# Kernel tuning notes

Measured on AMD Instinct MI355X. Metric: run time of the kernel, lower is better.

## Reference

```python
import jax, jax.numpy as jnp
import numpy as np

D_MODEL, D_K, D_V, H, GRID = 512, 64, 64, 8, 196
B = 4


def setup_inputs() -> dict:
    key = jax.random.key(0)
    ks = jax.random.split(key, 12)
    s = 0.02
    return {
        "queries": jax.random.normal(ks[0], (B, GRID, D_MODEL), jnp.float32),
        "keys": jax.random.normal(ks[1], (B, GRID, D_MODEL), jnp.float32),
        "values": jax.random.normal(ks[2], (B, GRID, D_MODEL), jnp.float32),
        "Wq": jax.random.normal(ks[3], (H * D_K, D_MODEL), jnp.float32) * s,
        "bq": jnp.zeros((H * D_K,), jnp.float32),
        "Wk": jax.random.normal(ks[4], (H * D_K, D_MODEL), jnp.float32) * s,
        "bk": jnp.zeros((H * D_K,), jnp.float32),
        "Wv": jax.random.normal(ks[5], (H * D_V, D_MODEL), jnp.float32) * s,
        "bv": jnp.zeros((H * D_V,), jnp.float32),
        "Wo": jax.random.normal(ks[6], (D_MODEL, H * D_V), jnp.float32) * s,
        "bo": jnp.zeros((D_MODEL,), jnp.float32),
        "scale": jnp.ones((1, H, GRID, GRID), jnp.float32) / np.sqrt(D_K).astype(np.float32),
    }


def reference(queries, keys, values, Wq, bq, Wk, bk, Wv, bv, Wo, bo, scale):
    b, nq, _ = queries.shape
    nk = values.shape[1]
    # linear projections (torch nn.Linear: x @ W.T + b)
    q_sig = queries @ Wq.T + bq          # (b, nq, h*dk)
    k_p = keys @ Wk.T + bk               # (b, nk, h*dk)
    v_p = values @ Wv.T + bv             # (b, nk, h*dv)
    # elementwise q*k interaction (b, nq, nk, h*dk)
    att_e = q_sig[:, :, None, :] * k_p[:, None, :, :]
    # sigmoid-gated values
    v_g = jax.nn.sigmoid(att_e) * v_p[:, None, :, :]
    v = v_g.reshape(b, nq, nk, H, D_K).transpose(0, 3, 1, 2, 4)      # (b,h,nq,nk,dk)
    att = att_e.reshape(b, nq, nk, H, D_K).transpose(0, 3, 1, 2, 4)  # (b,h,nq,nk,dk)
    att = att.sum(-1) * scale            # (b,h,nq,nk)
    p = jax.nn.softmax(att, axis=-1)     # dropout is identity in eval mode
    # (att.unsqueeze(-2) @ v).squeeze(-2)
    image = jnp.einsum("bhqk,bhqkd->bhqd", p, v)
    image = image.transpose(0, 2, 1, 3).reshape(b, nq, H * D_V)
    out = image @ Wo.T + bo              # (b, nq, d_model)
    out = jax.nn.sigmoid(q_sig * out) * out
    return out
```

## Files before the change

### kernel.cpp

```cpp
#include <hip/hip_runtime.h>
#include <hip/hip_bf16.h>
#include <math.h>

#define NQ 196
#define BATCH 4
#define HD 512
#define NH 8
#define DK 64
#define MROWS 784
#define MPAD 832

typedef __attribute__((ext_vector_type(8))) short short8;
typedef __attribute__((ext_vector_type(4))) float float4v;

__device__ __forceinline__ float b2f(short s) {
  return __uint_as_float(((unsigned)(unsigned short)s) << 16);
}
__device__ __forceinline__ short f2b(float x) {
  return __builtin_bit_cast(short, __float2bfloat16(x));
}
__device__ __forceinline__ float fexp2(float x) {
  float r; asm("v_exp_f32 %0, %1" : "=v"(r) : "v"(x)); return r;
}
__device__ __forceinline__ float frcp(float x) {
  float r; asm("v_rcp_f32 %0, %1" : "=v"(r) : "v"(x)); return r;
}

struct SplitArgs {
  const float* src[7];
  short* hi[7];
  short* lo[7];
};

__global__ __launch_bounds__(256)
void split_kernel(SplitArgs a) {
  const int blk = blockIdx.x;
  int seg, base;
  if (blk < 588) { seg = blk / 196; base = seg * 196; }
  else           { seg = 3 + (blk - 588) / 128; base = 588 + (seg - 3) * 128; }
  const size_t off = (size_t)(blk - base) * 2048 + (size_t)threadIdx.x * 8;
  const float* src = a.src[seg] + off;
  float4 v0 = *(const float4*)(src);
  float4 v1 = *(const float4*)(src + 4);
  float x[8] = {v0.x, v0.y, v0.z, v0.w, v1.x, v1.y, v1.z, v1.w};
  short hh[8], ll[8];
  #pragma unroll
  for (int i = 0; i < 8; ++i) {
    hh[i] = f2b(x[i]);
    ll[i] = f2b(x[i] - b2f(hh[i]));
  }
  short8 vh = {hh[0],hh[1],hh[2],hh[3],hh[4],hh[5],hh[6],hh[7]};
  short8 vl = {ll[0],ll[1],ll[2],ll[3],ll[4],ll[5],ll[6],ll[7]};
  *(short8*)(a.hi[seg] + off) = vh;
  *(short8*)(a.lo[seg] + off) = vl;
}

struct GemmZ {
  const short* Ah[3]; const short* Al[3];
  const short* Bh[3]; const short* Bl[3];
  const float* bias[3];
  float* Cf[3]; short* Ch[3]; short* Cl[3];
  const short* Gh; const short* Gl;
};

__global__ __launch_bounds__(256)
void mfma_gemm(GemmZ p, int M, int N, int K) {
  const int z = blockIdx.z;
  const short* __restrict__ Ah = p.Ah[z];
  const short* __restrict__ Al = p.Al[z];
  const short* __restrict__ Bh = p.Bh[z];
  const short* __restrict__ Bl = p.Bl[z];

  __shared__ short ldsA[2][2][32 * 32];
  __shared__ short ldsB[2][2][64 * 32];

  const int t = threadIdx.x;
  const int w = t >> 6, ln = t & 63;
  const int lm = ln & 15, quad = ln >> 4;
  const int m0 = blockIdx.x * 32, n0 = blockIdx.y * 64;

  const int aArr = t >> 7;
  const int aIdx = t & 127;
  const int aRow = aIdx >> 2, aK = (aIdx & 3) << 3;
  const int bRow = t >> 2,    bK = (t & 3) << 3;
  const short* __restrict__ Asrc = aArr ? Al : Ah;
  const size_t aoff = (size_t)(m0 + aRow) * K + aK;
  const size_t boff = (size_t)(n0 + bRow) * K + bK;

  const int wm = (w & 1) << 4, wn = (w >> 1) << 5;

  float4v acc[2] = {{0.f,0.f,0.f,0.f},{0.f,0.f,0.f,0.f}};

  short8 rA  = *(const short8*)(Asrc + aoff);
  short8 rBh = *(const short8*)(Bh + boff);
  short8 rBl = *(const short8*)(Bl + boff);

  const int T = K >> 5;
  for (int kt = 0; kt < T; ++kt) {
    const int buf = kt & 1;
    *(short8*)&ldsA[buf][aArr][aRow * 32 + aK] = rA;
    *(short8*)&ldsB[buf][0][bRow * 32 + bK]    = rBh;
    *(short8*)&ldsB[buf][1][bRow * 32 + bK]    = rBl;
    __syncthreads();
    if (kt + 1 < T) {
      rA  = *(const short8*)(Asrc + aoff + (size_t)(kt + 1) * 32);
      rBh = *(const short8*)(Bh + boff + (size_t)(kt + 1) * 32);
      rBl = *(const short8*)(Bl + boff + (size_t)(kt + 1) * 32);
    }
    short8 fah = *(const short8*)&ldsA[buf][0][(wm + lm) * 32 + (quad << 3)];
    short8 fal = *(const short8*)&ldsA[buf][1][(wm + lm) * 32 + (quad << 3)];
    #pragma unroll
    for (int ni = 0; ni < 2; ++ni) {
      short8 fbh = *(const short8*)&ldsB[buf][0][(wn + (ni << 4) + lm) * 32 + (quad << 3)];
      short8 fbl = *(const short8*)&ldsB[buf][1][(wn + (ni << 4) + lm) * 32 + (quad << 3)];
      acc[ni] = __builtin_amdgcn_mfma_f32_16x16x32_bf16(fah, fbh, acc[ni], 0,0,0);
      acc[ni] = __builtin_amdgcn_mfma_f32_16x16x32_bf16(fah, fbl, acc[ni], 0,0,0);
      acc[ni] = __builtin_amdgcn_mfma_f32_16x16x32_bf16(fal, fbh, acc[ni], 0,0,0);
    }
  }

  const float* bias = p.bias[z];
  float* Cf = p.Cf[z]; short* Ch = p.Ch[z]; short* Cl = p.Cl[z];
  #pragma unroll
  for (int ni = 0; ni < 2; ++ni) {
    const int n = n0 + wn + (ni << 4) + lm;
    const float bv = bias[n];
    #pragma unroll
    for (int r = 0; r < 4; ++r) {
      const int m = m0 + wm + (quad << 2) + r;
      if (m < M) {
        float c = acc[ni][r] + bv;
        if (p.Gh) {
          float qg = b2f(p.Gh[(size_t)m * N + n]) + b2f(p.Gl[(size_t)m * N + n]);
          c = __fdividef(c, 1.f + __expf(-qg * c));
        }
        if (Cf) Cf[(size_t)m * N + n] = c;
        if (Ch) {
          short hi = f2b(c);
          Ch[(size_t)m * N + n] = hi;
          Cl[(size_t)m * N + n] = f2b(c - b2f(hi));
        }
      }
    }
  }
}

__global__ __launch_bounds__(256)
void scores_softmax(const short* __restrict__ qsh, const short* __restrict__ qsl,
                    const short* __restrict__ ksh, const short* __restrict__ ksl,
                    const float* __restrict__ scg, float* __restrict__ pbuf) {
  const int q0 = blockIdx.x * 16;
  const int bh = blockIdx.y;
  const int b = bh >> 3, h = bh & 7;
  const int w = threadIdx.x >> 6, ln = threadIdx.x & 63;
  const int lm = ln & 15, quad = ln >> 4;
  const float L2E = 1.4426950408889634f;

  __shared__ float S[16][210];

  const size_t abase = ((size_t)(b * NQ) + q0 + lm) * HD + h * DK + (quad << 3);
  short8 ah0 = *(const short8*)(qsh + abase);
  short8 ah1 = *(const short8*)(qsh + abase + 32);
  short8 al0 = *(const short8*)(qsl + abase);
  short8 al1 = *(const short8*)(qsl + abase + 32);

  for (int nt = w; nt < 13; nt += 4) {
    const size_t bbase = ((size_t)(b * NQ) + nt * 16 + lm) * HD + h * DK + (quad << 3);
    short8 bh0 = *(const short8*)(ksh + bbase);
    short8 bh1 = *(const short8*)(ksh + bbase + 32);
    short8 bl0 = *(const short8*)(ksl + bbase);
    short8 bl1 = *(const short8*)(ksl + bbase + 32);
    float4v acc = {0.f, 0.f, 0.f, 0.f};
    acc = __builtin_amdgcn_mfma_f32_16x16x32_bf16(ah0, bh0, acc, 0,0,0);
    acc = __builtin_amdgcn_mfma_f32_16x16x32_bf16(ah1, bh1, acc, 0,0,0);
    acc = __builtin_amdgcn_mfma_f32_16x16x32_bf16(ah0, bl0, acc, 0,0,0);
    acc = __builtin_amdgcn_mfma_f32_16x16x32_bf16(ah1, bl1, acc, 0,0,0);
    acc = __builtin_amdgcn_mfma_f32_16x16x32_bf16(al0, bh0, acc, 0,0,0);
    acc = __builtin_amdgcn_mfma_f32_16x16x32_bf16(al1, bh1, acc, 0,0,0);
    #pragma unroll
    for (int r = 0; r < 4; ++r)
      S[(quad << 2) + r][nt * 16 + lm] = acc[r];
  }
  __syncthreads();

  for (int i = 0; i < 4; ++i) {
    const int rr = (w << 2) + i;
    const int q = q0 + rr;
    const bool qok = q < NQ;
    const float* srow = scg + ((size_t)h * NQ + (qok ? q : 0)) * NQ;
    float att[4];
    #pragma unroll
    for (int j = 0; j < 4; ++j) {
      const int c = ln + (j << 6);
      att[j] = -1e30f;
      if (c < NQ) att[j] = S[rr][c] * srow[c] * L2E;
    }
    float m = fmaxf(fmaxf(att[0], att[1]), fmaxf(att[2], att[3]));
    #pragma unroll
    for (int off = 32; off; off >>= 1) m = fmaxf(m, __shfl_xor(m, off, 64));
    float e[4], s = 0.f;
    #pragma unroll
    for (int j = 0; j < 4; ++j) { e[j] = fexp2(att[j] - m); s += e[j]; }
    #pragma unroll
    for (int off = 32; off; off >>= 1) s += __shfl_xor(s, off, 64);
    const float rinv = __fdividef(1.f, s);
    if (qok) {
      float* prow = pbuf + (((size_t)(b * NH + h) * NQ) + q) * NQ;
      #pragma unroll
      for (int j = 0; j < 4; ++j) {
        const int c = ln + (j << 6);
        if (c < NQ) prow[c] = e[j] * rinv;
      }
    }
  }
}

__global__ __launch_bounds__(512)
void pv_kernel(const short* __restrict__ qsh, const short* __restrict__ qsl,
               const float* __restrict__ kpg, const float* __restrict__ vpg,
               const float* __restrict__ pbuf, float* __restrict__ part) {
  const int b  = blockIdx.y;
  const int x  = blockIdx.x;
  const int ks = x & 3;
  const int q0 = (x >> 2) << 2;
  const int hd = threadIdx.x;
  const int h  = hd >> 6;
  const float LOG2E = 1.4426950408889634f;

  const size_t r0 = ((size_t)(b * NQ) + q0) * HD + hd;
  float nqs[4];
  #pragma unroll
  for (int qi = 0; qi < 4; ++qi) {
    const size_t rr = r0 + (size_t)qi * HD;
    nqs[qi] = -(b2f(qsh[rr]) + b2f(qsl[rr])) * LOG2E;
  }
  const float* kp = kpg + (size_t)b * NQ * HD + hd;
  const float* vp = vpg + (size_t)b * NQ * HD + hd;
  const float* pr = pbuf + ((size_t)(b * NH + h) * NQ + q0) * NQ;

  float acc[4] = {0.f, 0.f, 0.f, 0.f};
  const int kbeg = ks * 49;
  for (int k = kbeg; k < kbeg + 49; ++k) {
    const float kv = kp[(size_t)k * HD];
    const float vv = vp[(size_t)k * HD];
    #pragma unroll
    for (int qi = 0; qi < 4; ++qi) {
      const float e = fexp2(nqs[qi] * kv);
      const float g = vv * frcp(1.f + e);
      acc[qi] += pr[(size_t)qi * NQ + k] * g;
    }
  }
  float* dst = part + (size_t)ks * ((size_t)MROWS * HD) + r0;
  #pragma unroll
  for (int qi = 0; qi < 4; ++qi) dst[(size_t)qi * HD] = acc[qi];
}

__global__ __launch_bounds__(256)
void img_split(const float* __restrict__ part, short* __restrict__ ih,
               short* __restrict__ il) {
  const size_t NELF = (size_t)MROWS * HD;
  const size_t off = (size_t)blockIdx.x * 2048 + (size_t)threadIdx.x * 8;
  float x[8];
  #pragma unroll
  for (int i = 0; i < 8; i += 4) {
    float4 s0 = *(const float4*)(part + off + i);
    float4 s1 = *(const float4*)(part + NELF + off + i);
    float4 s2 = *(const float4*)(part + 2 * NELF + off + i);
    float4 s3 = *(const float4*)(part + 3 * NELF + off + i);
    x[i+0] = s0.x + s1.x + s2.x + s3.x;
    x[i+1] = s0.y + s1.y + s2.y + s3.y;
    x[i+2] = s0.z + s1.z + s2.z + s3.z;
    x[i+3] = s0.w + s1.w + s2.w + s3.w;
  }
  short hh[8], ll[8];
  #pragma unroll
  for (int i = 0; i < 8; ++i) {
    hh[i] = f2b(x[i]);
    ll[i] = f2b(x[i] - b2f(hh[i]));
  }
  short8 vh = {hh[0],hh[1],hh[2],hh[3],hh[4],hh[5],hh[6],hh[7]};
  short8 vl = {ll[0],ll[1],ll[2],ll[3],ll[4],ll[5],ll[6],ll[7]};
  *(short8*)(ih + off) = vh;
  *(short8*)(il + off) = vl;
}

extern "C" void kernel_launch(void* const* d_in, const int* in_sizes, int n_in,
                              void* d_out, int out_size, void* d_ws, size_t ws_size,
                              hipStream_t stream) {
  const float* queries = (const float*)d_in[0];
  const float* keys    = (const float*)d_in[1];
  const float* values  = (const float*)d_in[2];
  const float* Wq = (const float*)d_in[3];
  const float* bq = (const float*)d_in[4];
  const float* Wk = (const float*)d_in[5];
  const float* bk = (const float*)d_in[6];
  const float* Wv = (const float*)d_in[7];
  const float* bv = (const float*)d_in[8];
  const float* Wo = (const float*)d_in[9];
  const float* bo = (const float*)d_in[10];
  const float* scale = (const float*)d_in[11];

  char* base = (char*)d_ws;
  const size_t FB = sizeof(float);
  const size_t NELF  = (size_t)MROWS * HD;
  const size_t NELPS = (size_t)MPAD * HD;
  const size_t WEL   = (size_t)HD * HD;

  size_t o = 0;
  float* k_p  = (float*)(base + o); o += NELF * FB;
  float* v_p  = (float*)(base + o); o += NELF * FB;
  float* pbuf = (float*)(base + o); o += (size_t)BATCH * NH * NQ * NQ * FB;
  short* Wqh = (short*)(base + o); o += WEL * 2;
  short* Wql = (short*)(base + o); o += WEL * 2;
  short* Wkh = (short*)(base + o); o += WEL * 2;
  short* Wkl = (short*)(base + o); o += WEL * 2;
  short* Wvh = (short*)(base + o); o += WEL * 2;
  short* Wvl = (short*)(base + o); o += WEL * 2;
  short* Woh = (short*)(base + o); o += WEL * 2;
  short* Wol = (short*)(base + o); o += WEL * 2;
  short* qsh = (short*)(base + o); o += NELPS * 2;
  short* qsl = (short*)(base + o); o += NELPS * 2;
  short* ksh = (short*)(base + o); o += NELPS * 2;
  short* ksl = (short*)(base + o); o += NELPS * 2;
  char* regA = base + o;
  short* qh = (short*)(regA);
  short* ql = qh + NELPS; short* kh = ql + NELPS; short* kl = kh + NELPS;
  short* vh = kl + NELPS; short* vl = vh + NELPS;
  float* part  = (float*)(regA);
  short* imgh  = (short*)(part + 4 * NELF);
  short* imgl  = imgh + NELPS;

  SplitArgs sa;
  sa.src[0] = queries; sa.hi[0] = qh;  sa.lo[0] = ql;
  sa.src[1] = keys;    sa.hi[1] = kh;  sa.lo[1] = kl;
  sa.src[2] = values;  sa.hi[2] = vh;  sa.lo[2] = vl;
  sa.src[3] = Wq;      sa.hi[3] = Wqh; sa.lo[3] = Wql;
  sa.src[4] = Wk;      sa.hi[4] = Wkh; sa.lo[4] = Wkl;
  sa.src[5] = Wv;      sa.hi[5] = Wvh; sa.lo[5] = Wvl;
  sa.src[6] = Wo;      sa.hi[6] = Woh; sa.lo[6] = Wol;
  split_kernel<<<1100, 256, 0, stream>>>(sa);

  GemmZ gp;
  gp.Ah[0]=qh; gp.Al[0]=ql; gp.Bh[0]=Wqh; gp.Bl[0]=Wql; gp.bias[0]=bq;
  gp.Cf[0]=nullptr; gp.Ch[0]=qsh; gp.Cl[0]=qsl;
  gp.Ah[1]=kh; gp.Al[1]=kl; gp.Bh[1]=Wkh; gp.Bl[1]=Wkl; gp.bias[1]=bk;
  gp.Cf[1]=k_p; gp.Ch[1]=ksh; gp.Cl[1]=ksl;
  gp.Ah[2]=vh; gp.Al[2]=vl; gp.Bh[2]=Wvh; gp.Bl[2]=Wvl; gp.bias[2]=bv;
  gp.Cf[2]=v_p; gp.Ch[2]=nullptr; gp.Cl[2]=nullptr;
  gp.Gh = nullptr; gp.Gl = nullptr;
  mfma_gemm<<<dim3(25, HD/64, 3), 256, 0, stream>>>(gp, MROWS, HD, HD);

  scores_softmax<<<dim3(13, NH*BATCH), 256, 0, stream>>>(qsh, qsl, ksh, ksl, scale, pbuf);

  pv_kernel<<<dim3(196, BATCH), 512, 0, stream>>>(qsh, qsl, k_p, v_p, pbuf, part);

  img_split<<<MROWS*HD/2048, 256, 0, stream>>>(part, imgh, imgl);

  GemmZ go;
  go.Ah[0]=imgh; go.Al[0]=imgl; go.Bh[0]=Woh; go.Bl[0]=Wol; go.bias[0]=bo;
  go.Cf[0]=(float*)d_out; go.Ch[0]=nullptr; go.Cl[0]=nullptr;
  for (int i = 1; i < 3; ++i) {
    go.Ah[i]=nullptr; go.Al[i]=nullptr; go.Bh[i]=nullptr; go.Bl[i]=nullptr;
    go.bias[i]=nullptr; go.Cf[i]=nullptr; go.Ch[i]=nullptr; go.Cl[i]=nullptr;
  }
  go.Gh = qsh; go.Gl = qsl;
  mfma_gemm<<<dim3(25, HD/64, 1), 256, 0, stream>>>(go, MROWS, HD, HD);
}
```

Baseline: 148.5 us.

## Fuse bf16 hi/lo splitting and partial-sum reduction into GEMM loaders

Removes the standalone split kernel and the img_split kernel. The projection and output GEMMs now load fp32 inputs and weights directly and convert them to bf16 hi/lo inside the tile loader. The output GEMM also sums the four pv partial buffers while loading. q_sig is kept in fp32 for pv and the output gating. This saves two launches and the round trips through intermediate buffers, but weights are re-converted by every block, and each output-GEMM tile reads four partial buffers.

```diff
diff --git a/kernel.cpp b/kernel.cpp
--- a/kernel.cpp
+++ b/kernel.cpp
@@ -11,6 +11,7 @@
 #define MPAD 832
 
 typedef __attribute__((ext_vector_type(8))) short short8;
+typedef __attribute__((ext_vector_type(4))) short short4v;
 typedef __attribute__((ext_vector_type(4))) float float4v;
 
 __device__ __forceinline__ float b2f(short s) {
@@ -25,51 +26,25 @@
 __device__ __forceinline__ float frcp(float x) {
   float r; asm("v_rcp_f32 %0, %1" : "=v"(r) : "v"(x)); return r;
 }
-
-struct SplitArgs {
-  const float* src[7];
-  short* hi[7];
-  short* lo[7];
+__device__ __forceinline__ void cvt4(float4 v, short4v& hi, short4v& lo) {
+  float x[4] = {v.x, v.y, v.z, v.w};
+  #pragma unroll
+  for (int i = 0; i < 4; ++i) {
+    hi[i] = f2b(x[i]);
+    lo[i] = f2b(x[i] - b2f(hi[i]));
+  }
+}
+
+struct ProjArgs {
+  const float* X[3]; const float* W[3]; const float* bias[3];
+  float* Cf[3]; short* Ch[3]; short* Cl[3];
 };
 
 __global__ __launch_bounds__(256)
-void split_kernel(SplitArgs a) {
-  const int blk = blockIdx.x;
-  int seg, base;
-  if (blk < 588) { seg = blk / 196; base = seg * 196; }
-  else           { seg = 3 + (blk - 588) / 128; base = 588 + (seg - 3) * 128; }
-  const size_t off = (size_t)(blk - base) * 2048 + (size_t)threadIdx.x * 8;
-  const float* src = a.src[seg] + off;
-  float4 v0 = *(const float4*)(src);
-  float4 v1 = *(const float4*)(src + 4);
-  float x[8] = {v0.x, v0.y, v0.z, v0.w, v1.x, v1.y, v1.z, v1.w};
-  short hh[8], ll[8];
-  #pragma unroll
-  for (int i = 0; i < 8; ++i) {
-    hh[i] = f2b(x[i]);
-    ll[i] = f2b(x[i] - b2f(hh[i]));
-  }
-  short8 vh = {hh[0],hh[1],hh[2],hh[3],hh[4],hh[5],hh[6],hh[7]};
-  short8 vl = {ll[0],ll[1],ll[2],ll[3],ll[4],ll[5],ll[6],ll[7]};
-  *(short8*)(a.hi[seg] + off) = vh;
-  *(short8*)(a.lo[seg] + off) = vl;
-}
-
-struct GemmZ {
-  const short* Ah[3]; const short* Al[3];
-  const short* Bh[3]; const short* Bl[3];
-  const float* bias[3];
-  float* Cf[3]; short* Ch[3]; short* Cl[3];
-  const short* Gh; const short* Gl;
-};
-
-__global__ __launch_bounds__(256)
-void mfma_gemm(GemmZ p, int M, int N, int K) {
+void proj_gemm(ProjArgs p, int M, int N, int K) {
   const int z = blockIdx.z;
-  const short* __restrict__ Ah = p.Ah[z];
-  const short* __restrict__ Al = p.Al[z];
-  const short* __restrict__ Bh = p.Bh[z];
-  const short* __restrict__ Bl = p.Bl[z];
+  const float* __restrict__ X = p.X[z];
+  const float* __restrict__ W = p.W[z];
 
   __shared__ short ldsA[2][2][32 * 32];
   __shared__ short ldsB[2][2][64 * 32];
@@ -79,33 +54,35 @@
   const int lm = ln & 15, quad = ln >> 4;
   const int m0 = blockIdx.x * 32, n0 = blockIdx.y * 64;
 
-  const int aArr = t >> 7;
-  const int aIdx = t & 127;
-  const int aRow = aIdx >> 2, aK = (aIdx & 3) << 3;
-  const int bRow = t >> 2,    bK = (t & 3) << 3;
-  const short* __restrict__ Asrc = aArr ? Al : Ah;
-  const size_t aoff = (size_t)(m0 + aRow) * K + aK;
-  const size_t boff = (size_t)(n0 + bRow) * K + bK;
+  const int aRow = t >> 3, aK = (t & 7) << 2;
+  const int bRow = t >> 2, bK = (t & 3) << 3;
+  const int ar = min(m0 + aRow, M - 1);
+  const float* Ap = X + (size_t)ar * K + aK;
+  const float* Bp = W + (size_t)(n0 + bRow) * K + bK;
 
   const int wm = (w & 1) << 4, wn = (w >> 1) << 5;
-
   float4v acc[2] = {{0.f,0.f,0.f,0.f},{0.f,0.f,0.f,0.f}};
 
-  short8 rA  = *(const short8*)(Asrc + aoff);
-  short8 rBh = *(const short8*)(Bh + boff);
-  short8 rBl = *(const short8*)(Bl + boff);
+  float4 ra  = *(const float4*)Ap;
+  float4 rb0 = *(const float4*)Bp;
+  float4 rb1 = *(const float4*)(Bp + 4);
 
   const int T = K >> 5;
   for (int kt = 0; kt < T; ++kt) {
     const int buf = kt & 1;
-    *(short8*)&ldsA[buf][aArr][aRow * 32 + aK] = rA;
-    *(short8*)&ldsB[buf][0][bRow * 32 + bK]    = rBh;
-    *(short8*)&ldsB[buf][1][bRow * 32 + bK]    = rBl;
+    short4v ahi, alo; cvt4(ra, ahi, alo);
+    short4v bh0, bl0, bh1, bl1; cvt4(rb0, bh0, bl0); cvt4(rb1, bh1, bl1);
+    *(short4v*)&ldsA[buf][0][aRow * 32 + aK] = ahi;
+    *(short4v*)&ldsA[buf][1][aRow * 32 + aK] = alo;
+    short8 bh = {bh0[0],bh0[1],bh0[2],bh0[3],bh1[0],bh1[1],bh1[2],bh1[3]};
+    short8 bl = {bl0[0],bl0[1],bl0[2],bl0[3],bl1[0],bl1[1],bl1[2],bl1[3]};
+    *(short8*)&ldsB[buf][0][bRow * 32 + bK] = bh;
+    *(short8*)&ldsB[buf][1][bRow * 32 + bK] = bl;
     __syncthreads();
     if (kt + 1 < T) {
-      rA  = *(const short8*)(Asrc + aoff + (size_t)(kt + 1) * 32);
-      rBh = *(const short8*)(Bh + boff + (size_t)(kt + 1) * 32);
-      rBl = *(const short8*)(Bl + boff + (size_t)(kt + 1) * 32);
+      ra  = *(const float4*)(Ap + (size_t)(kt + 1) * 32);
+      rb0 = *(const float4*)(Bp + (size_t)(kt + 1) * 32);
+      rb1 = *(const float4*)(Bp + (size_t)(kt + 1) * 32 + 4);
     }
     short8 fah = *(const short8*)&ldsA[buf][0][(wm + lm) * 32 + (quad << 3)];
     short8 fal = *(const short8*)&ldsA[buf][1][(wm + lm) * 32 + (quad << 3)];
@@ -129,17 +106,94 @@
     for (int r = 0; r < 4; ++r) {
       const int m = m0 + wm + (quad << 2) + r;
       if (m < M) {
-        float c = acc[ni][r] + bv;
-        if (p.Gh) {
-          float qg = b2f(p.Gh[(size_t)m * N + n]) + b2f(p.Gl[(size_t)m * N + n]);
-          c = __fdividef(c, 1.f + __expf(-qg * c));
-        }
+        const float c = acc[ni][r] + bv;
         if (Cf) Cf[(size_t)m * N + n] = c;
         if (Ch) {
-          short hi = f2b(c);
+          const short hi = f2b(c);
           Ch[(size_t)m * N + n] = hi;
           Cl[(size_t)m * N + n] = f2b(c - b2f(hi));
         }
+      }
+    }
+  }
+}
+
+__global__ __launch_bounds__(256)
+void out_gemm(const float* __restrict__ part, const float* __restrict__ W,
+              const float* __restrict__ bias, const float* __restrict__ qsg,
+              float* __restrict__ C, int M, int N, int K) {
+  __shared__ short ldsA[2][2][32 * 32];
+  __shared__ short ldsB[2][2][64 * 32];
+
+  const int t = threadIdx.x;
+  const int w = t >> 6, ln = t & 63;
+  const int lm = ln & 15, quad = ln >> 4;
+  const int m0 = blockIdx.x * 32, n0 = blockIdx.y * 64;
+
+  const int aRow = t >> 3, aK = (t & 7) << 2;
+  const int bRow = t >> 2, bK = (t & 3) << 3;
+  const int ar = min(m0 + aRow, M - 1);
+  const size_t NELF = (size_t)MROWS * HD;
+  const float* Ap = part + (size_t)ar * K + aK;
+  const float* Bp = W + (size_t)(n0 + bRow) * K + bK;
+
+  const int wm = (w & 1) << 4, wn = (w >> 1) << 5;
+  float4v acc[2] = {{0.f,0.f,0.f,0.f},{0.f,0.f,0.f,0.f}};
+
+  float4 s0 = *(const float4*)(Ap);
+  float4 s1 = *(const float4*)(Ap + NELF);
+  float4 s2 = *(const float4*)(Ap + 2 * NELF);
+  float4 s3 = *(const float4*)(Ap + 3 * NELF);
+  float4 rb0 = *(const float4*)Bp;
+  float4 rb1 = *(const float4*)(Bp + 4);
+
+  const int T = K >> 5;
+  for (int kt = 0; kt < T; ++kt) {
+    const int buf = kt & 1;
+    float4 ra = make_float4(s0.x+s1.x+s2.x+s3.x, s0.y+s1.y+s2.y+s3.y,
+                            s0.z+s1.z+s2.z+s3.z, s0.w+s1.w+s2.w+s3.w);
+    short4v ahi, alo; cvt4(ra, ahi, alo);
+    short4v bh0, bl0, bh1, bl1; cvt4(rb0, bh0, bl0); cvt4(rb1, bh1, bl1);
+    *(short4v*)&ldsA[buf][0][aRow * 32 + aK] = ahi;
+    *(short4v*)&ldsA[buf][1][aRow * 32 + aK] = alo;
+    short8 bh = {bh0[0],bh0[1],bh0[2],bh0[3],bh1[0],bh1[1],bh1[2],bh1[3]};
+    short8 bl = {bl0[0],bl0[1],bl0[2],bl0[3],bl1[0],bl1[1],bl1[2],bl1[3]};
+    *(short8*)&ldsB[buf][0][bRow * 32 + bK] = bh;
+    *(short8*)&ldsB[buf][1][bRow * 32 + bK] = bl;
+    __syncthreads();
+    if (kt + 1 < T) {
+      const size_t ko = (size_t)(kt + 1) * 32;
+      s0 = *(const float4*)(Ap + ko);
+      s1 = *(const float4*)(Ap + NELF + ko);
+      s2 = *(const float4*)(Ap + 2 * NELF + ko);
+      s3 = *(const float4*)(Ap + 3 * NELF + ko);
+      rb0 = *(const float4*)(Bp + ko);
+      rb1 = *(const float4*)(Bp + ko + 4);
+    }
+    short8 fah = *(const short8*)&ldsA[buf][0][(wm + lm) * 32 + (quad << 3)];
+    short8 fal = *(const short8*)&ldsA[buf][1][(wm + lm) * 32 + (quad << 3)];
+    #pragma unroll
+    for (int ni = 0; ni < 2; ++ni) {
+      short8 fbh = *(const short8*)&ldsB[buf][0][(wn + (ni << 4) + lm) * 32 + (quad << 3)];
+      short8 fbl = *(const short8*)&ldsB[buf][1][(wn + (ni << 4) + lm) * 32 + (quad << 3)];
+      acc[ni] = __builtin_amdgcn_mfma_f32_16x16x32_bf16(fah, fbh, acc[ni], 0,0,0);
+      acc[ni] = __builtin_amdgcn_mfma_f32_16x16x32_bf16(fah, fbl, acc[ni], 0,0,0);
+      acc[ni] = __builtin_amdgcn_mfma_f32_16x16x32_bf16(fal, fbh, acc[ni], 0,0,0);
+    }
+  }
+
+  #pragma unroll
+  for (int ni = 0; ni < 2; ++ni) {
+    const int n = n0 + wn + (ni << 4) + lm;
+    const float bv = bias[n];
+    #pragma unroll
+    for (int r = 0; r < 4; ++r) {
+      const int m = m0 + wm + (quad << 2) + r;
+      if (m < M) {
+        float c = acc[ni][r] + bv;
+        const float qg = qsg[(size_t)m * N + n];
+        c = __fdividef(c, 1.f + __expf(-qg * c));
+        C[(size_t)m * N + n] = c;
       }
     }
   }
@@ -216,9 +270,9 @@
 }
 
 __global__ __launch_bounds__(512)
-void pv_kernel(const short* __restrict__ qsh, const short* __restrict__ qsl,
-               const float* __restrict__ kpg, const float* __restrict__ vpg,
-               const float* __restrict__ pbuf, float* __restrict__ part) {
+void pv_kernel(const float* __restrict__ qsg, const float* __restrict__ kpg,
+               const float* __restrict__ vpg, const float* __restrict__ pbuf,
+               float* __restrict__ part) {
   const int b  = blockIdx.y;
   const int x  = blockIdx.x;
   const int ks = x & 3;
@@ -230,10 +284,9 @@
   const size_t r0 = ((size_t)(b * NQ) + q0) * HD + hd;
   float nqs[4];
   #pragma unroll
-  for (int qi = 0; qi < 4; ++qi) {
-    const size_t rr = r0 + (size_t)qi * HD;
-    nqs[qi] = -(b2f(qsh[rr]) + b2f(qsl[rr])) * LOG2E;
-  }
+  for (int qi = 0; qi < 4; ++qi)
+    nqs[qi] = -qsg[r0 + (size_t)qi * HD] * LOG2E;
+
   const float* kp = kpg + (size_t)b * NQ * HD + hd;
   const float* vp = vpg + (size_t)b * NQ * HD + hd;
   const float* pr = pbuf + ((size_t)(b * NH + h) * NQ + q0) * NQ;
@@ -253,35 +306,6 @@
   float* dst = part + (size_t)ks * ((size_t)MROWS * HD) + r0;
   #pragma unroll
   for (int qi = 0; qi < 4; ++qi) dst[(size_t)qi * HD] = acc[qi];
-}
-
-__global__ __launch_bounds__(256)
-void img_split(const float* __restrict__ part, short* __restrict__ ih,
-               short* __restrict__ il) {
-  const size_t NELF = (size_t)MROWS * HD;
-  const size_t off = (size_t)blockIdx.x * 2048 + (size_t)threadIdx.x * 8;
-  float x[8];
-  #pragma unroll
-  for (int i = 0; i < 8; i += 4) {
-    float4 s0 = *(const float4*)(part + off + i);
-    float4 s1 = *(const float4*)(part + NELF + off + i);
-    float4 s2 = *(const float4*)(part + 2 * NELF + off + i);
-    float4 s3 = *(const float4*)(part + 3 * NELF + off + i);
-    x[i+0] = s0.x + s1.x + s2.x + s3.x;
-    x[i+1] = s0.y + s1.y + s2.y + s3.y;
-    x[i+2] = s0.z + s1.z + s2.z + s3.z;
-    x[i+3] = s0.w + s1.w + s2.w + s3.w;
-  }
-  short hh[8], ll[8];
-  #pragma unroll
-  for (int i = 0; i < 8; ++i) {
-    hh[i] = f2b(x[i]);
-    ll[i] = f2b(x[i] - b2f(hh[i]));
-  }
-  short8 vh = {hh[0],hh[1],hh[2],hh[3],hh[4],hh[5],hh[6],hh[7]};
-  short8 vl = {ll[0],ll[1],ll[2],ll[3],ll[4],ll[5],ll[6],ll[7]};
-  *(short8*)(ih + off) = vh;
-  *(short8*)(il + off) = vl;
 }
 
 extern "C" void kernel_launch(void* const* d_in, const int* in_sizes, int n_in,
@@ -304,65 +328,31 @@
   const size_t FB = sizeof(float);
   const size_t NELF  = (size_t)MROWS * HD;
   const size_t NELPS = (size_t)MPAD * HD;
-  const size_t WEL   = (size_t)HD * HD;
 
   size_t o = 0;
-  float* k_p  = (float*)(base + o); o += NELF * FB;
-  float* v_p  = (float*)(base + o); o += NELF * FB;
-  float* pbuf = (float*)(base + o); o += (size_t)BATCH * NH * NQ * NQ * FB;
-  short* Wqh = (short*)(base + o); o += WEL * 2;
-  short* Wql = (short*)(base + o); o += WEL * 2;
-  short* Wkh = (short*)(base + o); o += WEL * 2;
-  short* Wkl = (short*)(base + o); o += WEL * 2;
-  short* Wvh = (short*)(base + o); o += WEL * 2;
-  short* Wvl = (short*)(base + o); o += WEL * 2;
-  short* Woh = (short*)(base + o); o += WEL * 2;
-  short* Wol = (short*)(base + o); o += WEL * 2;
+  float* q_sig = (float*)(base + o); o += NELF * FB;
+  float* k_p   = (float*)(base + o); o += NELF * FB;
+  float* v_p   = (float*)(base + o); o += NELF * FB;
+  float* pbuf  = (float*)(base + o); o += (size_t)BATCH * NH * NQ * NQ * FB;
   short* qsh = (short*)(base + o); o += NELPS * 2;
   short* qsl = (short*)(base + o); o += NELPS * 2;
   short* ksh = (short*)(base + o); o += NELPS * 2;
   short* ksl = (short*)(base + o); o += NELPS * 2;
-  char* regA = base + o;
-  short* qh = (short*)(regA);
-  short* ql = qh + NELPS; short* kh = ql + NELPS; short* kl = kh + NELPS;
-  short* vh = kl + NELPS; short* vl = vh + NELPS;
-  float* part  = (float*)(regA);
-  short* imgh  = (short*)(part + 4 * NELF);
-  short* imgl  = imgh + NELPS;
-
-  SplitArgs sa;
-  sa.src[0] = queries; sa.hi[0] = qh;  sa.lo[0] = ql;
-  sa.src[1] = keys;    sa.hi[1] = kh;  sa.lo[1] = kl;
-  sa.src[2] = values;  sa.hi[2] = vh;  sa.lo[2] = vl;
-  sa.src[3] = Wq;      sa.hi[3] = Wqh; sa.lo[3] = Wql;
-  sa.src[4] = Wk;      sa.hi[4] = Wkh; sa.lo[4] = Wkl;
-  sa.src[5] = Wv;      sa.hi[5] = Wvh; sa.lo[5] = Wvl;
-  sa.src[6] = Wo;      sa.hi[6] = Woh; sa.lo[6] = Wol;
-  split_kernel<<<1100, 256, 0, stream>>>(sa);
-
-  GemmZ gp;
-  gp.Ah[0]=qh; gp.Al[0]=ql; gp.Bh[0]=Wqh; gp.Bl[0]=Wql; gp.bias[0]=bq;
-  gp.Cf[0]=nullptr; gp.Ch[0]=qsh; gp.Cl[0]=qsl;
-  gp.Ah[1]=kh; gp.Al[1]=kl; gp.Bh[1]=Wkh; gp.Bl[1]=Wkl; gp.bias[1]=bk;
-  gp.Cf[1]=k_p; gp.Ch[1]=ksh; gp.Cl[1]=ksl;
-  gp.Ah[2]=vh; gp.Al[2]=vl; gp.Bh[2]=Wvh; gp.Bl[2]=Wvl; gp.bias[2]=bv;
-  gp.Cf[2]=v_p; gp.Ch[2]=nullptr; gp.Cl[2]=nullptr;
-  gp.Gh = nullptr; gp.Gl = nullptr;
-  mfma_gemm<<<dim3(25, HD/64, 3), 256, 0, stream>>>(gp, MROWS, HD, HD);
+  float* part = (float*)(base + o); o += 4 * NELF * FB;
+
+  ProjArgs gp;
+  gp.X[0] = queries; gp.W[0] = Wq; gp.bias[0] = bq;
+  gp.Cf[0] = q_sig;  gp.Ch[0] = qsh; gp.Cl[0] = qsl;
+  gp.X[1] = keys;    gp.W[1] = Wk; gp.bias[1] = bk;
+  gp.Cf[1] = k_p;    gp.Ch[1] = ksh; gp.Cl[1] = ksl;
+  gp.X[2] = values;  gp.W[2] = Wv; gp.bias[2] = bv;
+  gp.Cf[2] = v_p;    gp.Ch[2] = nullptr; gp.Cl[2] = nullptr;
+  proj_gemm<<<dim3(25, HD/64, 3), 256, 0, stream>>>(gp, MROWS, HD, HD);
 
   scores_softmax<<<dim3(13, NH*BATCH), 256, 0, stream>>>(qsh, qsl, ksh, ksl, scale, pbuf);
 
-  pv_kernel<<<dim3(196, BATCH), 512, 0, stream>>>(qsh, qsl, k_p, v_p, pbuf, part);
-
-  img_split<<<MROWS*HD/2048, 256, 0, stream>>>(part, imgh, imgl);
-
-  GemmZ go;
-  go.Ah[0]=imgh; go.Al[0]=imgl; go.Bh[0]=Woh; go.Bl[0]=Wol; go.bias[0]=bo;
-  go.Cf[0]=(float*)d_out; go.Ch[0]=nullptr; go.Cl[0]=nullptr;
-  for (int i = 1; i < 3; ++i) {
-    go.Ah[i]=nullptr; go.Al[i]=nullptr; go.Bh[i]=nullptr; go.Bl[i]=nullptr;
-    go.bias[i]=nullptr; go.Cf[i]=nullptr; go.Ch[i]=nullptr; go.Cl[i]=nullptr;
-  }
-  go.Gh = qsh; go.Gl = qsl;
-  mfma_gemm<<<dim3(25, HD/64, 1), 256, 0, stream>>>(go, MROWS, HD, HD);
-}
+  pv_kernel<<<dim3(196, BATCH), 512, 0, stream>>>(q_sig, k_p, v_p, pbuf, part);
+
+  out_gemm<<<dim3(25, HD/64, 1), 256, 0, stream>>>(part, Wo, bo, q_sig,
+                                                   (float*)d_out, MROWS, HD, HD);
+}
```

Result: faster. 144.1 us (-2.9%).
